# Performance work log

Measured on AMD Instinct MI355X. Metric: run time of the kernel, lower is better.

## Reference

```python
import jax, jax.numpy as jnp
import numpy as np

C_Z, H, C = 128, 4, 32
L = 320
SCALE = 1.0 / np.sqrt(C)
EPS = 1e-5


def setup_inputs() -> dict:
    key = jax.random.key(0)
    ks = jax.random.split(key, 8)
    s = 0.02
    return {
        "z": jax.random.normal(ks[0], (L, L, C_Z), dtype=jnp.float32),
        "pair_mask": jnp.ones((L, L), dtype=jnp.float32),
        "res_mask": jnp.ones((L,), dtype=bool),
        "ln_gamma": jnp.ones((C_Z,), dtype=jnp.float32),
        "ln_beta": jnp.zeros((C_Z,), dtype=jnp.float32),
        "Wq": jax.random.normal(ks[1], (C_Z, H * C), dtype=jnp.float32) * s,
        "Wk": jax.random.normal(ks[2], (C_Z, H * C), dtype=jnp.float32) * s,
        "Wv": jax.random.normal(ks[3], (C_Z, H * C), dtype=jnp.float32) * s,
        "Wb": jax.random.normal(ks[4], (C_Z, H), dtype=jnp.float32) * s,
        "Wg": jax.random.normal(ks[5], (C_Z, H * C), dtype=jnp.float32) * s,
        "Wout": jax.random.normal(ks[6], (H * C, C_Z), dtype=jnp.float32) * s,
    }


def _layernorm(x, gamma, beta):
    mu = jnp.mean(x, axis=-1, keepdims=True)
    var = jnp.mean(jnp.square(x - mu), axis=-1, keepdims=True)
    return (x - mu) * jax.lax.rsqrt(var + EPS) * gamma + beta


def reference(z, pair_mask, res_mask, ln_gamma, ln_beta, Wq, Wk, Wv, Wb, Wg, Wout):
    Ldim = z.shape[0]
    z_ln = _layernorm(z, ln_gamma, ln_beta)                      # [L,L,c_z]
    Q = (z_ln @ Wq).reshape(Ldim, Ldim, H, C)                    # [i,j,h,c]
    K = (z_ln @ Wk).reshape(Ldim, Ldim, H, C)                    # [i,k,h,c]
    V = (z_ln @ Wv).reshape(Ldim, Ldim, H, C)                    # [i,k,h,c]
    B = z_ln @ Wb                                                # [j,k,h]
    G = jax.nn.sigmoid(z_ln @ Wg).reshape(Ldim, Ldim, H, C)      # [i,j,h,c]

    # logits[i,h,j,k] = <Q[i,j], K[i,k]> * scale + B[j,k,h]
    logits = jnp.einsum("ijhc,ikhc->ihjk", Q, K) * SCALE
    logits = logits + jnp.transpose(B, (2, 0, 1))[None]          # +[1,h,j,k]
    neg_inf = jnp.asarray(-jnp.inf, logits.dtype)
    logits = jnp.where(res_mask[None, None, None, :], logits, neg_inf)
    attn = jax.nn.softmax(logits, axis=-1)                       # over k

    out = jnp.einsum("ihjk,ikhc->ijhc", attn, V)                 # [i,j,h,c]
    out = (G * out).reshape(Ldim, Ldim, H * C)
    dz = out @ Wout                                              # [L,L,c_z]
    return dz * pair_mask[..., None]
```

## Files before the change

### kernel.cpp

```cpp
#include <hip/hip_runtime.h>

#define LDIM 320
#define CZ 128
#define NH 4
#define CH 32
#define SCALE_QK 0.17677669529663687f
#define LN_EPS 1e-5f

typedef __attribute__((ext_vector_type(8))) short bf16x8;
typedef __attribute__((ext_vector_type(4))) float f32x4;

__device__ __forceinline__ unsigned int pack_bf2(float a, float b) {
  unsigned int ua = __float_as_uint(a);
  unsigned int ub = __float_as_uint(b);
  unsigned int ra = (ua + 0x7fffu + ((ua >> 16) & 1u)) >> 16;
  unsigned int rb = (ub + 0x7fffu + ((ub >> 16) & 1u)) >> 16;
  return (ra & 0xffffu) | (rb << 16);
}

__device__ __forceinline__ unsigned short f2bf(float a) {
  unsigned int ua = __float_as_uint(a);
  return (unsigned short)((ua + 0x7fffu + ((ua >> 16) & 1u)) >> 16);
}

__device__ __forceinline__ float bf2f(unsigned short u) {
  return __uint_as_float(((unsigned int)u) << 16);
}

__global__ __launch_bounds__(256) void k_prep(
    const float* __restrict__ Wq, const float* __restrict__ Wk,
    const float* __restrict__ Wv, const float* __restrict__ Wb,
    const float* __restrict__ Wg, const float* __restrict__ Wout,
    unsigned short* __restrict__ Wt, unsigned short* __restrict__ Woutt)
{
  __shared__ __attribute__((aligned(16))) unsigned short buf[64 * 136];
  const int t = threadIdx.x, bid = blockIdx.x;
  const bool isOut = (bid >= 9);
  const int n0 = isOut ? (bid - 9) * 64 : bid * 64;
  const int nl = t & 63;
  const int n = n0 + nl;
#pragma unroll 8
  for (int it = 0; it < 32; ++it) {
    const int k = (t >> 6) + 4 * it;
    float v;
    if (isOut)        v = Wout[k * 128 + n];
    else if (n < 128) v = Wq[k * 128 + n];
    else if (n < 256) v = Wk[k * 128 + n - 128];
    else if (n < 384) v = Wv[k * 128 + n - 256];
    else if (n < 512) v = Wg[k * 128 + n - 384];
    else if (n < 516) v = Wb[k * 4 + n - 512];
    else              v = 0.f;
    buf[nl * 136 + k] = f2bf(v);
  }
  __syncthreads();
  unsigned short* dst = isOut ? Woutt : Wt;
#pragma unroll
  for (int it = 0; it < 4; ++it) {
    const int idx = t + 256 * it;
    const int rr = idx >> 4, ck = idx & 15;
    const uint4 d = *(const uint4*)&buf[rr * 136 + ck * 8];
    *(uint4*)(dst + (size_t)(n0 + rr) * 128 + ck * 8) = d;
  }
}

__global__ __launch_bounds__(256) void k_lnproj(
    const float* __restrict__ z, const float* __restrict__ gamma,
    const float* __restrict__ beta, const unsigned short* __restrict__ Wt,
    unsigned short* __restrict__ Qg, unsigned short* __restrict__ Kg,
    unsigned short* __restrict__ Vg, unsigned short* __restrict__ Gg,
    float* __restrict__ Bh)
{
  __shared__ __attribute__((aligned(16))) unsigned short As[128 * 136];
  __shared__ __attribute__((aligned(16))) unsigned short Bs[64 * 136];
  const int t = threadIdx.x;
  const int ntile = blockIdx.x;
  const int m0 = blockIdx.y * 128;

  {
    const int r = t >> 1, half = t & 1;
    float x[64];
    const float* zp = z + (size_t)(m0 + r) * CZ + half * 64;
    float s = 0.f, ss = 0.f;
#pragma unroll
    for (int ii = 0; ii < 16; ++ii) {
      const float4 v = *(const float4*)(zp + ii * 4);
      x[ii * 4 + 0] = v.x; x[ii * 4 + 1] = v.y;
      x[ii * 4 + 2] = v.z; x[ii * 4 + 3] = v.w;
      s += v.x + v.y + v.z + v.w;
      ss += v.x * v.x + v.y * v.y + v.z * v.z + v.w * v.w;
    }
    s  += __shfl_xor(s, 1);
    ss += __shfl_xor(ss, 1);
    const float mu  = s * (1.f / 128.f);
    const float var = ss * (1.f / 128.f) - mu * mu;
    const float rs  = rsqrtf(var + LN_EPS);
    const float* gp = gamma + half * 64;
    const float* bp = beta + half * 64;
    unsigned int* As32 = (unsigned int*)As;
    const int dbase = r * 68 + half * 32;
#pragma unroll
    for (int q = 0; q < 8; ++q) {
      const float4 g0 = *(const float4*)(gp + q * 8);
      const float4 g1 = *(const float4*)(gp + q * 8 + 4);
      const float4 b0 = *(const float4*)(bp + q * 8);
      const float4 b1 = *(const float4*)(bp + q * 8 + 4);
      const float y0 = (x[q * 8 + 0] - mu) * rs * g0.x + b0.x;
      const float y1 = (x[q * 8 + 1] - mu) * rs * g0.y + b0.y;
      const float y2 = (x[q * 8 + 2] - mu) * rs * g0.z + b0.z;
      const float y3 = (x[q * 8 + 3] - mu) * rs * g0.w + b0.w;
      const float y4 = (x[q * 8 + 4] - mu) * rs * g1.x + b1.x;
      const float y5 = (x[q * 8 + 5] - mu) * rs * g1.y + b1.y;
      const float y6 = (x[q * 8 + 6] - mu) * rs * g1.z + b1.z;
      const float y7 = (x[q * 8 + 7] - mu) * rs * g1.w + b1.w;
      uint4 u;
      u.x = pack_bf2(y0, y1); u.y = pack_bf2(y2, y3);
      u.z = pack_bf2(y4, y5); u.w = pack_bf2(y6, y7);
      *(uint4*)&As32[dbase + q * 4] = u;
    }
  }
  {
    const unsigned short* wrow = Wt + (size_t)ntile * 64 * 128;
#pragma unroll
    for (int it = 0; it < 4; ++it) {
      const int idx = t + 256 * it;
      const int n = idx >> 4, ck = idx & 15;
      const uint4 d = *(const uint4*)(wrow + n * 128 + ck * 8);
      *(uint4*)&Bs[n * 136 + ck * 8] = d;
    }
  }
  __syncthreads();

  const int w = t >> 6, lane = t & 63;
  const int m16 = lane & 15, qd = lane >> 4;
  const f32x4 z4 = {0.f, 0.f, 0.f, 0.f};
  f32x4 acc[2][4];
#pragma unroll
  for (int sub = 0; sub < 2; ++sub)
#pragma unroll
    for (int nt = 0; nt < 4; ++nt) acc[sub][nt] = z4;

#pragma unroll
  for (int ks = 0; ks < 4; ++ks) {
    const bf16x8 af0 = *(const bf16x8*)&As[(w * 32 + m16) * 136 + qd * 8 + ks * 32];
    const bf16x8 af1 = *(const bf16x8*)&As[(w * 32 + 16 + m16) * 136 + qd * 8 + ks * 32];
#pragma unroll
    for (int nt = 0; nt < 4; ++nt) {
      const bf16x8 bf = *(const bf16x8*)&Bs[(nt * 16 + m16) * 136 + qd * 8 + ks * 32];
      acc[0][nt] = __builtin_amdgcn_mfma_f32_16x16x32_bf16(af0, bf, acc[0][nt], 0, 0, 0);
      acc[1][nt] = __builtin_amdgcn_mfma_f32_16x16x32_bf16(af1, bf, acc[1][nt], 0, 0, 0);
    }
  }

#pragma unroll
  for (int sub = 0; sub < 2; ++sub) {
#pragma unroll
    for (int r = 0; r < 4; ++r) {
      const int p = m0 + w * 32 + sub * 16 + qd * 4 + r;
      const int a = p / 320, bb = p - a * 320;
      if (ntile < 8) {
#pragma unroll
        for (int nt = 0; nt < 4; ++nt) {
          const int n = ntile * 64 + nt * 16 + m16;
          const int off = n & 127, hh = off >> 5, cc = off & 31;
          float val = acc[sub][nt][r];
          if (ntile >= 6) val = 1.f / (1.f + __expf(-val));
          unsigned short* dst =
              (ntile < 2 ? Qg : (ntile < 4 ? Kg : (ntile < 6 ? Vg : Gg)));
          dst[((size_t)(a * 4 + hh) * 320 + bb) * 32 + cc] = f2bf(val);
        }
      } else {
        if (m16 < 4) Bh[(size_t)m16 * 102400 + p] = acc[sub][0][r];
      }
    }
  }
}

__global__ __launch_bounds__(256) void k_attn(
    const unsigned short* __restrict__ Qg, const unsigned short* __restrict__ Kg,
    const unsigned short* __restrict__ Vg, const unsigned short* __restrict__ Gg,
    const float* __restrict__ Bh, const int* __restrict__ rmask,
    unsigned short* __restrict__ Obg)
{
  __shared__ __attribute__((aligned(16))) unsigned short Vt[32 * 328];
  __shared__ __attribute__((aligned(16))) unsigned short Ps[4][16 * 168];
  const int h = blockIdx.x, i = blockIdx.y;
  const int t = threadIdx.x;
  const size_t base = (size_t)(i * NH + h) * (LDIM * CH);

  {
    const int k0 = t >> 3, c4 = (t & 7) * 4;
#pragma unroll
    for (int it = 0; it < 10; ++it) {
      const int k = k0 + 32 * it;
      const uint2 d = *(const uint2*)(Vg + base + k * 32 + c4);
      Vt[(c4 + 0) * 328 + k] = (unsigned short)(d.x & 0xffffu);
      Vt[(c4 + 1) * 328 + k] = (unsigned short)(d.x >> 16);
      Vt[(c4 + 2) * 328 + k] = (unsigned short)(d.y & 0xffffu);
      Vt[(c4 + 3) * 328 + k] = (unsigned short)(d.y >> 16);
    }
  }
  __syncthreads();

  const int w = t >> 6, lane = t & 63;
  const int m16 = lane & 15, qd = lane >> 4;
  const f32x4 z4 = {0.f, 0.f, 0.f, 0.f};

  float mkr[20];
#pragma unroll
  for (int kt = 0; kt < 20; ++kt)
    mkr[kt] = rmask[kt * 16 + m16] ? 0.f : -INFINITY;

  for (int jt = w; jt < 20; jt += 4) {
    const bf16x8 qfrag =
        *(const bf16x8*)(Qg + base + (size_t)(jt * 16 + m16) * 32 + qd * 8);

    f32x4 acc[20];
#pragma unroll
    for (int kt = 0; kt < 20; ++kt) {
      const bf16x8 kf =
          *(const bf16x8*)(Kg + base + (size_t)(kt * 16 + m16) * 32 + qd * 8);
      acc[kt] = __builtin_amdgcn_mfma_f32_16x16x32_bf16(qfrag, kf, z4, 0, 0, 0);
    }

    const float* bp = Bh + (size_t)h * 102400 +
                      (size_t)(jt * 16 + qd * 4) * 320 + m16;
    float mx[4] = {-INFINITY, -INFINITY, -INFINITY, -INFINITY};
#pragma unroll
    for (int kt = 0; kt < 20; ++kt) {
#pragma unroll
      for (int r = 0; r < 4; ++r) {
        const float b = bp[r * 320 + kt * 16];
        const float s = fmaf(acc[kt][r], SCALE_QK, b) + mkr[kt];
        acc[kt][r] = s;
        mx[r] = fmaxf(mx[r], s);
      }
    }
#pragma unroll
    for (int r = 0; r < 4; ++r) {
      mx[r] = fmaxf(mx[r], __shfl_xor(mx[r], 1));
      mx[r] = fmaxf(mx[r], __shfl_xor(mx[r], 2));
      mx[r] = fmaxf(mx[r], __shfl_xor(mx[r], 4));
      mx[r] = fmaxf(mx[r], __shfl_xor(mx[r], 8));
    }
    float l[4] = {0.f, 0.f, 0.f, 0.f};
#pragma unroll
    for (int kt = 0; kt < 20; ++kt) {
#pragma unroll
      for (int r = 0; r < 4; ++r) {
        const float p = __expf(acc[kt][r] - mx[r]);
        acc[kt][r] = p;
        l[r] += p;
      }
    }
#pragma unroll
    for (int r = 0; r < 4; ++r) {
      l[r] += __shfl_xor(l[r], 1);
      l[r] += __shfl_xor(l[r], 2);
      l[r] += __shfl_xor(l[r], 4);
      l[r] += __shfl_xor(l[r], 8);
    }
    float rl[4];
#pragma unroll
    for (int r = 0; r < 4; ++r) rl[r] = 1.f / l[r];

    f32x4 accO0 = z4, accO1 = z4;
#pragma unroll
    for (int hh = 0; hh < 2; ++hh) {
      __syncthreads();
#pragma unroll
      for (int kt2 = 0; kt2 < 10; ++kt2) {
        const int kt = hh * 10 + kt2;
#pragma unroll
        for (int r = 0; r < 4; ++r)
          Ps[w][(qd * 4 + r) * 168 + kt2 * 16 + m16] = f2bf(acc[kt][r] * rl[r]);
      }
      __syncthreads();
#pragma unroll
      for (int ks = 0; ks < 5; ++ks) {
        const bf16x8 pf = *(const bf16x8*)&Ps[w][m16 * 168 + ks * 32 + qd * 8];
        const bf16x8 v0 =
            *(const bf16x8*)&Vt[m16 * 328 + hh * 160 + ks * 32 + qd * 8];
        const bf16x8 v1 =
            *(const bf16x8*)&Vt[(16 + m16) * 328 + hh * 160 + ks * 32 + qd * 8];
        accO0 = __builtin_amdgcn_mfma_f32_16x16x32_bf16(pf, v0, accO0, 0, 0, 0);
        accO1 = __builtin_amdgcn_mfma_f32_16x16x32_bf16(pf, v1, accO1, 0, 0, 0);
      }
    }

#pragma unroll
    for (int r = 0; r < 4; ++r) {
      const int j = jt * 16 + qd * 4 + r;
      const float g0 = bf2f(Gg[base + (size_t)j * 32 + m16]);
      const float g1 = bf2f(Gg[base + (size_t)j * 32 + 16 + m16]);
      unsigned short* op = Obg + (size_t)(i * 320 + j) * 128 + h * 32;
      op[m16]      = f2bf(g0 * accO0[r]);
      op[16 + m16] = f2bf(g1 * accO1[r]);
    }
  }
}

__global__ __launch_bounds__(256) void k_out(
    const unsigned short* __restrict__ Obg, const unsigned short* __restrict__ Woutt,
    const float* __restrict__ pm, float* __restrict__ out)
{
  __shared__ __attribute__((aligned(16))) unsigned short As[128 * 136];
  __shared__ __attribute__((aligned(16))) unsigned short Bs[64 * 136];
  const int t = threadIdx.x;
  const int ntile = blockIdx.x;
  const int m0 = blockIdx.y * 128;

#pragma unroll
  for (int it = 0; it < 8; ++it) {
    const int idx = t + 256 * it;
    const int rr = idx >> 4, ck = idx & 15;
    const uint4 d = *(const uint4*)(Obg + (size_t)(m0 + rr) * 128 + ck * 8);
    *(uint4*)&As[rr * 136 + ck * 8] = d;
  }
  {
    const unsigned short* wrow = Woutt + (size_t)ntile * 64 * 128;
#pragma unroll
    for (int it = 0; it < 4; ++it) {
      const int idx = t + 256 * it;
      const int n = idx >> 4, ck = idx & 15;
      const uint4 d = *(const uint4*)(wrow + n * 128 + ck * 8);
      *(uint4*)&Bs[n * 136 + ck * 8] = d;
    }
  }
  __syncthreads();

  const int w = t >> 6, lane = t & 63;
  const int m16 = lane & 15, qd = lane >> 4;
  const f32x4 z4 = {0.f, 0.f, 0.f, 0.f};
  f32x4 acc[2][4];
#pragma unroll
  for (int sub = 0; sub < 2; ++sub)
#pragma unroll
    for (int nt = 0; nt < 4; ++nt) acc[sub][nt] = z4;

#pragma unroll
  for (int ks = 0; ks < 4; ++ks) {
    const bf16x8 af0 = *(const bf16x8*)&As[(w * 32 + m16) * 136 + qd * 8 + ks * 32];
    const bf16x8 af1 = *(const bf16x8*)&As[(w * 32 + 16 + m16) * 136 + qd * 8 + ks * 32];
#pragma unroll
    for (int nt = 0; nt < 4; ++nt) {
      const bf16x8 bf = *(const bf16x8*)&Bs[(nt * 16 + m16) * 136 + qd * 8 + ks * 32];
      acc[0][nt] = __builtin_amdgcn_mfma_f32_16x16x32_bf16(af0, bf, acc[0][nt], 0, 0, 0);
      acc[1][nt] = __builtin_amdgcn_mfma_f32_16x16x32_bf16(af1, bf, acc[1][nt], 0, 0, 0);
    }
  }

#pragma unroll
  for (int sub = 0; sub < 2; ++sub) {
#pragma unroll
    for (int r = 0; r < 4; ++r) {
      const int p = m0 + w * 32 + sub * 16 + qd * 4 + r;
      const float m = pm[p];
      float* orow = out + (size_t)p * 128 + ntile * 64;
#pragma unroll
      for (int nt = 0; nt < 4; ++nt)
        orow[nt * 16 + m16] = acc[sub][nt][r] * m;
    }
  }
}

extern "C" void kernel_launch(void* const* d_in, const int* in_sizes, int n_in,
                              void* d_out, int out_size, void* d_ws, size_t ws_size,
                              hipStream_t stream)
{
  const float* z     = (const float*)d_in[0];
  const float* pmask = (const float*)d_in[1];
  const int*   rmask = (const int*)d_in[2];
  const float* gamma = (const float*)d_in[3];
  const float* beta  = (const float*)d_in[4];
  const float* Wq    = (const float*)d_in[5];
  const float* Wk    = (const float*)d_in[6];
  const float* Wv    = (const float*)d_in[7];
  const float* Wb    = (const float*)d_in[8];
  const float* Wg    = (const float*)d_in[9];
  const float* Wout  = (const float*)d_in[10];

  const size_t P = (size_t)LDIM * LDIM;
  const size_t E = P * 128;
  char* ws = (char*)d_ws;
  unsigned short* Qg = (unsigned short*)ws;
  unsigned short* Kg = Qg + E;
  unsigned short* Vg = Kg + E;
  unsigned short* Gg = Vg + E;
  unsigned short* Obg = Gg + E;
  unsigned short* Wt = Obg + E;
  unsigned short* Woutt = Wt + 576 * 128;
  float* Bh = (float*)(Woutt + 128 * 128);

  k_prep<<<dim3(11), 256, 0, stream>>>(Wq, Wk, Wv, Wb, Wg, Wout, Wt, Woutt);
  k_lnproj<<<dim3(9, 800), 256, 0, stream>>>(z, gamma, beta, Wt,
                                             Qg, Kg, Vg, Gg, Bh);
  k_attn<<<dim3(NH, LDIM), 256, 0, stream>>>(Qg, Kg, Vg, Gg, Bh, rmask, Obg);
  k_out<<<dim3(2, 800), 256, 0, stream>>>(Obg, Woutt, pmask, (float*)d_out);
}
```

Before: 405.0 us.

## Compute layernorm once per row block and loop over all projection tiles

```diff
diff --git a/kernel.cpp b/kernel.cpp
--- a/kernel.cpp
+++ b/kernel.cpp
@@ -71,93 +71,89 @@
     float* __restrict__ Bh)
 {
   __shared__ __attribute__((aligned(16))) unsigned short As[128 * 136];
-  __shared__ __attribute__((aligned(16))) unsigned short Bs[64 * 136];
   const int t = threadIdx.x;
-  const int ntile = blockIdx.x;
-  const int m0 = blockIdx.y * 128;
-
-  {
-    const int r = t >> 1, half = t & 1;
-    float x[64];
-    const float* zp = z + (size_t)(m0 + r) * CZ + half * 64;
-    float s = 0.f, ss = 0.f;
-#pragma unroll
-    for (int ii = 0; ii < 16; ++ii) {
-      const float4 v = *(const float4*)(zp + ii * 4);
-      x[ii * 4 + 0] = v.x; x[ii * 4 + 1] = v.y;
-      x[ii * 4 + 2] = v.z; x[ii * 4 + 3] = v.w;
-      s += v.x + v.y + v.z + v.w;
-      ss += v.x * v.x + v.y * v.y + v.z * v.z + v.w * v.w;
-    }
-    s  += __shfl_xor(s, 1);
-    ss += __shfl_xor(ss, 1);
+  const int m0 = blockIdx.x * 128;
+  const int rlane = t & 7;
+
+  const float* gp = gamma + rlane * 16;
+  const float* bp = beta + rlane * 16;
+  const float4 g0 = *(const float4*)(gp + 0);
+  const float4 g1 = *(const float4*)(gp + 4);
+  const float4 g2 = *(const float4*)(gp + 8);
+  const float4 g3 = *(const float4*)(gp + 12);
+  const float4 b0 = *(const float4*)(bp + 0);
+  const float4 b1 = *(const float4*)(bp + 4);
+  const float4 b2 = *(const float4*)(bp + 8);
+  const float4 b3 = *(const float4*)(bp + 12);
+
+#pragma unroll
+  for (int rr = 0; rr < 4; ++rr) {
+    const int row = rr * 32 + (t >> 3);
+    const float* zp = z + (size_t)(m0 + row) * CZ + rlane * 16;
+    const float4 x0 = *(const float4*)(zp + 0);
+    const float4 x1 = *(const float4*)(zp + 4);
+    const float4 x2 = *(const float4*)(zp + 8);
+    const float4 x3 = *(const float4*)(zp + 12);
+    float s  = x0.x + x0.y + x0.z + x0.w + x1.x + x1.y + x1.z + x1.w +
+               x2.x + x2.y + x2.z + x2.w + x3.x + x3.y + x3.z + x3.w;
+    float ss = x0.x*x0.x + x0.y*x0.y + x0.z*x0.z + x0.w*x0.w +
+               x1.x*x1.x + x1.y*x1.y + x1.z*x1.z + x1.w*x1.w +
+               x2.x*x2.x + x2.y*x2.y + x2.z*x2.z + x2.w*x2.w +
+               x3.x*x3.x + x3.y*x3.y + x3.z*x3.z + x3.w*x3.w;
+    s  += __shfl_xor(s, 1);  ss += __shfl_xor(ss, 1);
+    s  += __shfl_xor(s, 2);  ss += __shfl_xor(ss, 2);
+    s  += __shfl_xor(s, 4);  ss += __shfl_xor(ss, 4);
     const float mu  = s * (1.f / 128.f);
     const float var = ss * (1.f / 128.f) - mu * mu;
     const float rs  = rsqrtf(var + LN_EPS);
-    const float* gp = gamma + half * 64;
-    const float* bp = beta + half * 64;
-    unsigned int* As32 = (unsigned int*)As;
-    const int dbase = r * 68 + half * 32;
-#pragma unroll
-    for (int q = 0; q < 8; ++q) {
-      const float4 g0 = *(const float4*)(gp + q * 8);
-      const float4 g1 = *(const float4*)(gp + q * 8 + 4);
-      const float4 b0 = *(const float4*)(bp + q * 8);
-      const float4 b1 = *(const float4*)(bp + q * 8 + 4);
-      const float y0 = (x[q * 8 + 0] - mu) * rs * g0.x + b0.x;
-      const float y1 = (x[q * 8 + 1] - mu) * rs * g0.y + b0.y;
-      const float y2 = (x[q * 8 + 2] - mu) * rs * g0.z + b0.z;
-      const float y3 = (x[q * 8 + 3] - mu) * rs * g0.w + b0.w;
-      const float y4 = (x[q * 8 + 4] - mu) * rs * g1.x + b1.x;
-      const float y5 = (x[q * 8 + 5] - mu) * rs * g1.y + b1.y;
-      const float y6 = (x[q * 8 + 6] - mu) * rs * g1.z + b1.z;
-      const float y7 = (x[q * 8 + 7] - mu) * rs * g1.w + b1.w;
-      uint4 u;
-      u.x = pack_bf2(y0, y1); u.y = pack_bf2(y2, y3);
-      u.z = pack_bf2(y4, y5); u.w = pack_bf2(y6, y7);
-      *(uint4*)&As32[dbase + q * 4] = u;
-    }
-  }
-  {
-    const unsigned short* wrow = Wt + (size_t)ntile * 64 * 128;
-#pragma unroll
-    for (int it = 0; it < 4; ++it) {
-      const int idx = t + 256 * it;
-      const int n = idx >> 4, ck = idx & 15;
-      const uint4 d = *(const uint4*)(wrow + n * 128 + ck * 8);
-      *(uint4*)&Bs[n * 136 + ck * 8] = d;
-    }
+    uint4 u0, u1;
+    u0.x = pack_bf2((x0.x - mu) * rs * g0.x + b0.x, (x0.y - mu) * rs * g0.y + b0.y);
+    u0.y = pack_bf2((x0.z - mu) * rs * g0.z + b0.z, (x0.w - mu) * rs * g0.w + b0.w);
+    u0.z = pack_bf2((x1.x - mu) * rs * g1.x + b1.x, (x1.y - mu) * rs * g1.y + b1.y);
+    u0.w = pack_bf2((x1.z - mu) * rs * g1.z + b1.z, (x1.w - mu) * rs * g1.w + b1.w);
+    u1.x = pack_bf2((x2.x - mu) * rs * g2.x + b2.x, (x2.y - mu) * rs * g2.y + b2.y);
+    u1.y = pack_bf2((x2.z - mu) * rs * g2.z + b2.z, (x2.w - mu) * rs * g2.w + b2.w);
+    u1.z = pack_bf2((x3.x - mu) * rs * g3.x + b3.x, (x3.y - mu) * rs * g3.y + b3.y);
+    u1.w = pack_bf2((x3.z - mu) * rs * g3.z + b3.z, (x3.w - mu) * rs * g3.w + b3.w);
+    unsigned short* dst = &As[row * 136 + rlane * 16];
+    *(uint4*)(dst + 0) = u0;
+    *(uint4*)(dst + 8) = u1;
   }
   __syncthreads();
 
   const int w = t >> 6, lane = t & 63;
   const int m16 = lane & 15, qd = lane >> 4;
   const f32x4 z4 = {0.f, 0.f, 0.f, 0.f};
-  f32x4 acc[2][4];
-#pragma unroll
-  for (int sub = 0; sub < 2; ++sub)
-#pragma unroll
-    for (int nt = 0; nt < 4; ++nt) acc[sub][nt] = z4;
-
+
+  bf16x8 af[2][4];
 #pragma unroll
   for (int ks = 0; ks < 4; ++ks) {
-    const bf16x8 af0 = *(const bf16x8*)&As[(w * 32 + m16) * 136 + qd * 8 + ks * 32];
-    const bf16x8 af1 = *(const bf16x8*)&As[(w * 32 + 16 + m16) * 136 + qd * 8 + ks * 32];
-#pragma unroll
-    for (int nt = 0; nt < 4; ++nt) {
-      const bf16x8 bf = *(const bf16x8*)&Bs[(nt * 16 + m16) * 136 + qd * 8 + ks * 32];
-      acc[0][nt] = __builtin_amdgcn_mfma_f32_16x16x32_bf16(af0, bf, acc[0][nt], 0, 0, 0);
-      acc[1][nt] = __builtin_amdgcn_mfma_f32_16x16x32_bf16(af1, bf, acc[1][nt], 0, 0, 0);
-    }
-  }
-
-#pragma unroll
-  for (int sub = 0; sub < 2; ++sub) {
-#pragma unroll
-    for (int r = 0; r < 4; ++r) {
-      const int p = m0 + w * 32 + sub * 16 + qd * 4 + r;
-      const int a = p / 320, bb = p - a * 320;
-      if (ntile < 8) {
+    af[0][ks] = *(const bf16x8*)&As[(w * 32 + m16) * 136 + ks * 32 + qd * 8];
+    af[1][ks] = *(const bf16x8*)&As[(w * 32 + 16 + m16) * 136 + ks * 32 + qd * 8];
+  }
+
+  for (int ntile = 0; ntile < 8; ++ntile) {
+    f32x4 acc[2][4];
+#pragma unroll
+    for (int sub = 0; sub < 2; ++sub)
+#pragma unroll
+      for (int nt = 0; nt < 4; ++nt) acc[sub][nt] = z4;
+#pragma unroll
+    for (int ks = 0; ks < 4; ++ks) {
+#pragma unroll
+      for (int nt = 0; nt < 4; ++nt) {
+        const bf16x8 bf = *(const bf16x8*)(
+            Wt + (size_t)(ntile * 64 + nt * 16 + m16) * 128 + ks * 32 + qd * 8);
+        acc[0][nt] = __builtin_amdgcn_mfma_f32_16x16x32_bf16(af[0][ks], bf, acc[0][nt], 0, 0, 0);
+        acc[1][nt] = __builtin_amdgcn_mfma_f32_16x16x32_bf16(af[1][ks], bf, acc[1][nt], 0, 0, 0);
+      }
+    }
+#pragma unroll
+    for (int sub = 0; sub < 2; ++sub) {
+#pragma unroll
+      for (int r = 0; r < 4; ++r) {
+        const int p = m0 + w * 32 + sub * 16 + qd * 4 + r;
+        const int a = p / 320, bb = p - a * 320;
 #pragma unroll
         for (int nt = 0; nt < 4; ++nt) {
           const int n = ntile * 64 + nt * 16 + m16;
@@ -168,8 +164,25 @@
               (ntile < 2 ? Qg : (ntile < 4 ? Kg : (ntile < 6 ? Vg : Gg)));
           dst[((size_t)(a * 4 + hh) * 320 + bb) * 32 + cc] = f2bf(val);
         }
-      } else {
-        if (m16 < 4) Bh[(size_t)m16 * 102400 + p] = acc[sub][0][r];
+      }
+    }
+  }
+
+  {
+    f32x4 acc0 = z4, acc1 = z4;
+#pragma unroll
+    for (int ks = 0; ks < 4; ++ks) {
+      const bf16x8 bf = *(const bf16x8*)(
+          Wt + (size_t)(512 + m16) * 128 + ks * 32 + qd * 8);
+      acc0 = __builtin_amdgcn_mfma_f32_16x16x32_bf16(af[0][ks], bf, acc0, 0, 0, 0);
+      acc1 = __builtin_amdgcn_mfma_f32_16x16x32_bf16(af[1][ks], bf, acc1, 0, 0, 0);
+    }
+    if (m16 < 4) {
+#pragma unroll
+      for (int r = 0; r < 4; ++r) {
+        const int p0 = m0 + w * 32 + qd * 4 + r;
+        Bh[(size_t)m16 * 102400 + p0] = acc0[r];
+        Bh[(size_t)m16 * 102400 + p0 + 16] = acc1[r];
       }
     }
   }
@@ -392,8 +405,8 @@
   float* Bh = (float*)(Woutt + 128 * 128);
 
   k_prep<<<dim3(11), 256, 0, stream>>>(Wq, Wk, Wv, Wb, Wg, Wout, Wt, Woutt);
-  k_lnproj<<<dim3(9, 800), 256, 0, stream>>>(z, gamma, beta, Wt,
-                                             Qg, Kg, Vg, Gg, Bh);
+  k_lnproj<<<dim3(800), 256, 0, stream>>>(z, gamma, beta, Wt,
+                                          Qg, Kg, Vg, Gg, Bh);
   k_attn<<<dim3(NH, LDIM), 256, 0, stream>>>(Qg, Kg, Vg, Gg, Bh, rmask, Obg);
   k_out<<<dim3(2, 800), 256, 0, stream>>>(Obg, Woutt, pmask, (float*)d_out);
 }
```

Measured after the change: 352.4 us. -13.0%, faster.
